# Kernel tuning notes

Hardware: AMD Instinct MI355X
Metric: run time of the kernel (lower is better)

The kernel has to match this reference:

```python
import jax, jax.numpy as jnp
import numpy as np


def setup_inputs() -> dict:
    key = jax.random.key(0)
    kx, ky = jax.random.split(key)
    B, N, M, D = 32, 1024, 1024, 256
    x = jax.random.normal(kx, (B, N, D), dtype=jnp.float32)
    y = jax.random.normal(ky, (B, M, D), dtype=jnp.float32)
    return {"x": x, "y": y}


def reference(x, y):
    # Faithful to torch: M = bmm(x, y^T) [B,N,M]; rowsum over dim=1 -> [B,M];
    # colsum over dim=2 -> [B,N]; concat -> [B, M+N].
    scores = jnp.einsum("bnd,bmd->bnm", x, y)  # [B,N,M]
    rowsum = scores.sum(axis=1)  # [B,M]
    colsum = scores.sum(axis=2)  # [B,N]
    return jnp.concatenate((rowsum, colsum), axis=1)
```

## Files before the change

kernel.cpp:

```cpp
#include <hip/hip_runtime.h>

#define BB 32
#define NN 1024
#define DD 256
#define SPLIT 8
#define CHUNK (NN / SPLIT)

__global__ void colsum_partial_kernel(const float* __restrict__ x,
                                      const float* __restrict__ y,
                                      float* __restrict__ partial) {
    int bid = blockIdx.x;
    int t   = bid / (BB * SPLIT);
    int rem = bid % (BB * SPLIT);
    int b   = rem / SPLIT;
    int s   = rem % SPLIT;
    int d   = threadIdx.x;

    const float* src = (t == 0 ? x : y)
                     + (size_t)b * NN * DD + (size_t)s * CHUNK * DD + d;

    float a0 = 0.f, a1 = 0.f, a2 = 0.f, a3 = 0.f;
    #pragma unroll 4
    for (int n = 0; n < CHUNK; n += 4) {
        a0 += src[(size_t)(n + 0) * DD];
        a1 += src[(size_t)(n + 1) * DD];
        a2 += src[(size_t)(n + 2) * DD];
        a3 += src[(size_t)(n + 3) * DD];
    }
    partial[(((size_t)t * SPLIT + s) * BB + b) * DD + d] = (a0 + a1) + (a2 + a3);
}

#define RCHUNKS 16
#define ROWS_PER_BLOCK 64

__global__ void dots_kernel(const float* __restrict__ x,
                            const float* __restrict__ y,
                            const float* __restrict__ partial,
                            float* __restrict__ out) {
    int bid = blockIdx.x;
    int rc  = bid % RCHUNKS;
    int bt  = bid / RCHUNKS;
    int t   = bt & 1;
    int b   = bt >> 1;
    int d   = threadIdx.x;

    __shared__ float ssum[DD];

    {
        const float* p = partial + ((size_t)t * SPLIT * BB + b) * DD + d;
        float s = 0.f;
        #pragma unroll
        for (int k = 0; k < SPLIT; ++k) s += p[(size_t)k * BB * DD];
        ssum[d] = s;
    }
    __syncthreads();

    int lane = threadIdx.x & 63;
    int wave = threadIdx.x >> 6;

    float4 sv = *reinterpret_cast<const float4*>(&ssum[lane * 4]);

    const float* data = (t == 0 ? y : x) + (size_t)b * NN * DD;
    float* outp = out + (size_t)b * 2048 + (size_t)t * 1024;

    int row0 = rc * ROWS_PER_BLOCK + wave * 16;
    #pragma unroll 4
    for (int r = 0; r < 16; ++r) {
        int row = row0 + r;
        float4 v = *reinterpret_cast<const float4*>(&data[(size_t)row * DD + lane * 4]);
        float dotv = v.x * sv.x + v.y * sv.y + v.z * sv.z + v.w * sv.w;
        #pragma unroll
        for (int off = 32; off >= 1; off >>= 1)
            dotv += __shfl_down(dotv, off, 64);
        if (lane == 0) outp[row] = dotv;
    }
}

extern "C" void kernel_launch(void* const* d_in, const int* in_sizes, int n_in,
                              void* d_out, int out_size, void* d_ws, size_t ws_size,
                              hipStream_t stream) {
    const float* x = (const float*)d_in[0];
    const float* y = (const float*)d_in[1];
    float* out     = (float*)d_out;
    float* partial = (float*)d_ws;

    colsum_partial_kernel<<<2 * BB * SPLIT, 256, 0, stream>>>(x, y, partial);
    dots_kernel<<<BB * 2 * RCHUNKS, 256, 0, stream>>>(x, y, partial, out);
}
```

Before: 26.78 us.

## Fuse colsum and dot kernels into one cooperative kernel with grid sync

Replaces the two-kernel pipeline with one cooperative kernel. Each block loads its 64 rows into registers once, computes partial column sums, then waits on a grid-wide barrier. After the barrier it computes dot products against the opposite tensor's column sums, reusing the rows already held in registers. This halves global reads of x and y and removes one launch, at the cost of grid sync overhead, high register use (16 float4 per thread), and the requirement that all 1024 blocks be co-resident. If the occupancy check fails, it falls back to the old two-kernel path.

```diff
diff --git a/kernel.cpp b/kernel.cpp
--- a/kernel.cpp
+++ b/kernel.cpp
@@ -1,8 +1,73 @@
 #include <hip/hip_runtime.h>
+#include <hip/hip_cooperative_groups.h>
+
+namespace cg = cooperative_groups;
 
 #define BB 32
 #define NN 1024
 #define DD 256
+
+#define NSLICE 64
+#define BPS 16
+#define NBLOCKS (NSLICE * BPS)
+#define RPB 64
+#define RPW 16
+
+__global__ __launch_bounds__(256, 4)
+void fused_kernel(const float* __restrict__ x, const float* __restrict__ y,
+                  float* __restrict__ partial,
+                  float* __restrict__ out) {
+    const int bid   = blockIdx.x;
+    const int slice = bid / BPS;
+    const int chunk = bid % BPS;
+    const int t     = slice >> 5;
+    const int b     = slice & 31;
+    const int lane  = threadIdx.x & 63;
+    const int wave  = threadIdx.x >> 6;
+    const int d     = threadIdx.x;
+
+    const int row0 = chunk * RPB + wave * RPW;
+    const float4* srcv = reinterpret_cast<const float4*>(
+        (t == 0 ? x : y) + (size_t)b * NN * DD) + (size_t)row0 * (DD / 4) + lane;
+
+    float4 v[RPW];
+    float4 p = make_float4(0.f, 0.f, 0.f, 0.f);
+    #pragma unroll
+    for (int r = 0; r < RPW; ++r) {
+        v[r] = srcv[(size_t)r * (DD / 4)];
+        p.x += v[r].x; p.y += v[r].y; p.z += v[r].z; p.w += v[r].w;
+    }
+
+    __shared__ float lds[4][DD];
+    *reinterpret_cast<float4*>(&lds[wave][lane * 4]) = p;
+    __syncthreads();
+    float ps = lds[0][d] + lds[1][d] + lds[2][d] + lds[3][d];
+    partial[((size_t)chunk * NSLICE + slice) * DD + d] = ps;
+
+    __threadfence();
+    cg::this_grid().sync();
+
+    const int opp = slice ^ 32;
+    const float* pp = partial + (size_t)opp * DD + d;
+    float s = 0.f;
+    #pragma unroll
+    for (int k = 0; k < BPS; ++k) s += pp[(size_t)k * NSLICE * DD];
+    lds[0][d] = s;
+    __syncthreads();
+
+    const float4 sv = *reinterpret_cast<const float4*>(&lds[0][lane * 4]);
+
+    float* outp = out + (size_t)b * 2048 + (t == 0 ? 1024 : 0) + row0;
+    #pragma unroll
+    for (int r = 0; r < RPW; ++r) {
+        float dv = v[r].x * sv.x + v[r].y * sv.y + v[r].z * sv.z + v[r].w * sv.w;
+        #pragma unroll
+        for (int off = 32; off >= 1; off >>= 1)
+            dv += __shfl_down(dv, off, 64);
+        if (lane == 0) outp[r] = dv;
+    }
+}
+
 #define SPLIT 8
 #define CHUNK (NN / SPLIT)
 
@@ -45,7 +110,6 @@
     int d   = threadIdx.x;
 
     __shared__ float ssum[DD];
-
     {
         const float* p = partial + ((size_t)t * SPLIT * BB + b) * DD + d;
         float s = 0.f;
@@ -59,16 +123,15 @@
     int wave = threadIdx.x >> 6;
 
     float4 sv = *reinterpret_cast<const float4*>(&ssum[lane * 4]);
-
     const float* data = (t == 0 ? y : x) + (size_t)b * NN * DD;
     float* outp = out + (size_t)b * 2048 + (size_t)t * 1024;
 
-    int row0 = rc * ROWS_PER_BLOCK + wave * 16;
+    int r0 = rc * ROWS_PER_BLOCK + wave * 16;
     #pragma unroll 4
     for (int r = 0; r < 16; ++r) {
-        int row = row0 + r;
-        float4 v = *reinterpret_cast<const float4*>(&data[(size_t)row * DD + lane * 4]);
-        float dotv = v.x * sv.x + v.y * sv.y + v.z * sv.z + v.w * sv.w;
+        int row = r0 + r;
+        float4 w = *reinterpret_cast<const float4*>(&data[(size_t)row * DD + lane * 4]);
+        float dotv = w.x * sv.x + w.y * sv.y + w.z * sv.z + w.w * sv.w;
         #pragma unroll
         for (int off = 32; off >= 1; off >>= 1)
             dotv += __shfl_down(dotv, off, 64);
@@ -84,6 +147,22 @@
     float* out     = (float*)d_out;
     float* partial = (float*)d_ws;
 
+    static int use_coop = -1;
+    if (use_coop < 0) {
+        int nb = 0;
+        hipError_t e = hipOccupancyMaxActiveBlocksPerMultiprocessor(
+            &nb, (const void*)fused_kernel, 256, 0);
+        use_coop = (e == hipSuccess && nb >= 4) ? 1 : 0;
+    }
+
+    if (use_coop) {
+        void* args[] = { (void*)&x, (void*)&y, (void*)&partial, (void*)&out };
+        hipError_t e = hipLaunchCooperativeKernel(
+            (const void*)fused_kernel, dim3(NBLOCKS), dim3(256), args, 0, stream);
+        if (e == hipSuccess) return;
+        use_coop = 0;
+    }
+
     colsum_partial_kernel<<<2 * BB * SPLIT, 256, 0, stream>>>(x, y, partial);
     dots_kernel<<<BB * 2 * RCHUNKS, 256, 0, stream>>>(x, y, partial, out);
 }
```

New measurement: 32.18 us. +20.2%, slower.

## Reduce column sums with float4 wave partials and atomics, removing split partials

Applied to the files above, without the earlier changes.

The column-sum pass now uses 1024 blocks, each summing 64 rows with float4 loads per wave. Partials are combined in LDS and atomically added into a single sum vector per slice, instead of 8 split partials that the dot kernel later re-summed. The dot kernel now reads one precomputed vector and keeps the same block mapping as the sum kernel, which may improve cache locality. In exchange it adds a memset launch and atomic traffic, and the float summation order is no longer deterministic.

```diff
diff --git a/kernel.cpp b/kernel.cpp
--- a/kernel.cpp
+++ b/kernel.cpp
@@ -3,76 +3,80 @@
 #define BB 32
 #define NN 1024
 #define DD 256
-#define SPLIT 8
-#define CHUNK (NN / SPLIT)
 
-__global__ void colsum_partial_kernel(const float* __restrict__ x,
-                                      const float* __restrict__ y,
-                                      float* __restrict__ partial) {
-    int bid = blockIdx.x;
-    int t   = bid / (BB * SPLIT);
-    int rem = bid % (BB * SPLIT);
-    int b   = rem / SPLIT;
-    int s   = rem % SPLIT;
-    int d   = threadIdx.x;
+#define NSLICE 64
+#define BPS 16
+#define NBLOCKS (NSLICE * BPS)
+#define RPB 64
+#define RPW 16
 
-    const float* src = (t == 0 ? x : y)
-                     + (size_t)b * NN * DD + (size_t)s * CHUNK * DD + d;
+#define WS_FSUM_BYTES (NSLICE * DD * 4)
 
-    float a0 = 0.f, a1 = 0.f, a2 = 0.f, a3 = 0.f;
-    #pragma unroll 4
-    for (int n = 0; n < CHUNK; n += 4) {
-        a0 += src[(size_t)(n + 0) * DD];
-        a1 += src[(size_t)(n + 1) * DD];
-        a2 += src[(size_t)(n + 2) * DD];
-        a3 += src[(size_t)(n + 3) * DD];
+__global__ __launch_bounds__(256)
+void sum_kernel(const float* __restrict__ x, const float* __restrict__ y,
+                float* __restrict__ fsum) {
+    const int bid   = blockIdx.x;
+    const int slice = bid / BPS;
+    const int chunk = bid % BPS;
+    const int t     = slice >> 5;
+    const int b     = slice & 31;
+    const int lane  = threadIdx.x & 63;
+    const int wave  = threadIdx.x >> 6;
+    const int d     = threadIdx.x;
+
+    const int row0 = chunk * RPB + wave * RPW;
+    const float4* srcv = reinterpret_cast<const float4*>(
+        (t == 0 ? x : y) + (size_t)b * NN * DD) + (size_t)row0 * (DD / 4) + lane;
+
+    float4 p = make_float4(0.f, 0.f, 0.f, 0.f);
+    #pragma unroll
+    for (int r = 0; r < RPW; ++r) {
+        float4 v = srcv[(size_t)r * (DD / 4)];
+        p.x += v.x; p.y += v.y; p.z += v.z; p.w += v.w;
     }
-    partial[(((size_t)t * SPLIT + s) * BB + b) * DD + d] = (a0 + a1) + (a2 + a3);
+
+    __shared__ float lds[4][DD];
+    *reinterpret_cast<float4*>(&lds[wave][lane * 4]) = p;
+    __syncthreads();
+    float ps = lds[0][d] + lds[1][d] + lds[2][d] + lds[3][d];
+
+    __hip_atomic_fetch_add(&fsum[(size_t)slice * DD + d], ps,
+                           __ATOMIC_RELAXED, __HIP_MEMORY_SCOPE_AGENT);
 }
 
-#define RCHUNKS 16
-#define ROWS_PER_BLOCK 64
-
-__global__ void dots_kernel(const float* __restrict__ x,
-                            const float* __restrict__ y,
-                            const float* __restrict__ partial,
-                            float* __restrict__ out) {
-    int bid = blockIdx.x;
-    int rc  = bid % RCHUNKS;
-    int bt  = bid / RCHUNKS;
-    int t   = bt & 1;
-    int b   = bt >> 1;
-    int d   = threadIdx.x;
+__global__ __launch_bounds__(256)
+void dots2_kernel(const float* __restrict__ x, const float* __restrict__ y,
+                  const float* __restrict__ fsum,
+                  float* __restrict__ out) {
+    const int bid   = blockIdx.x;
+    const int slice = bid / BPS;
+    const int chunk = bid % BPS;
+    const int t     = slice >> 5;
+    const int b     = slice & 31;
+    const int lane  = threadIdx.x & 63;
+    const int wave  = threadIdx.x >> 6;
+    const int d     = threadIdx.x;
+    const int opp   = slice ^ 32;
 
     __shared__ float ssum[DD];
-
-    {
-        const float* p = partial + ((size_t)t * SPLIT * BB + b) * DD + d;
-        float s = 0.f;
-        #pragma unroll
-        for (int k = 0; k < SPLIT; ++k) s += p[(size_t)k * BB * DD];
-        ssum[d] = s;
-    }
+    ssum[d] = fsum[(size_t)opp * DD + d];
     __syncthreads();
 
-    int lane = threadIdx.x & 63;
-    int wave = threadIdx.x >> 6;
+    const float4 sv = *reinterpret_cast<const float4*>(&ssum[lane * 4]);
 
-    float4 sv = *reinterpret_cast<const float4*>(&ssum[lane * 4]);
+    const float* data = (t == 0 ? x : y) + (size_t)b * NN * DD;
+    float* outp = out + (size_t)b * 2048 + (t == 0 ? 1024 : 0);
 
-    const float* data = (t == 0 ? y : x) + (size_t)b * NN * DD;
-    float* outp = out + (size_t)b * 2048 + (size_t)t * 1024;
-
-    int row0 = rc * ROWS_PER_BLOCK + wave * 16;
+    const int row0 = chunk * RPB + wave * RPW;
     #pragma unroll 4
-    for (int r = 0; r < 16; ++r) {
-        int row = row0 + r;
+    for (int r = 0; r < RPW; ++r) {
+        const int row = row0 + r;
         float4 v = *reinterpret_cast<const float4*>(&data[(size_t)row * DD + lane * 4]);
-        float dotv = v.x * sv.x + v.y * sv.y + v.z * sv.z + v.w * sv.w;
+        float dv = v.x * sv.x + v.y * sv.y + v.z * sv.z + v.w * sv.w;
         #pragma unroll
         for (int off = 32; off >= 1; off >>= 1)
-            dotv += __shfl_down(dotv, off, 64);
-        if (lane == 0) outp[row] = dotv;
+            dv += __shfl_down(dv, off, 64);
+        if (lane == 0) outp[row] = dv;
     }
 }
 
@@ -82,8 +86,9 @@
     const float* x = (const float*)d_in[0];
     const float* y = (const float*)d_in[1];
     float* out     = (float*)d_out;
-    float* partial = (float*)d_ws;
+    float* fsum    = (float*)d_ws;
 
-    colsum_partial_kernel<<<2 * BB * SPLIT, 256, 0, stream>>>(x, y, partial);
-    dots_kernel<<<BB * 2 * RCHUNKS, 256, 0, stream>>>(x, y, partial, out);
+    hipMemsetAsync(fsum, 0, WS_FSUM_BYTES, stream);
+    sum_kernel<<<NBLOCKS, 256, 0, stream>>>(x, y, fsum);
+    dots2_kernel<<<NBLOCKS, 256, 0, stream>>>(x, y, fsum, out);
 }
```

After: 34.59 us. +29.2%, slower.
